# Kernel tuning notes

Hardware: AMD Instinct MI355X
Metric: run time of the kernel (lower is better)

The kernel has to match this reference:

```python
import jax, jax.numpy as jnp
import numpy as np

N_THRESHOLDS = 10


def setup_inputs() -> dict:
    key = jax.random.key(0)
    k1, k2, k3 = jax.random.split(key, 3)
    shape = (32, 1024, 1024)
    prediction = jax.random.normal(k1, shape, dtype=jnp.float32)
    mask = jax.random.randint(k2, shape, 0, 2, dtype=jnp.int32)
    target = jax.random.randint(k3, shape, 0, 2, dtype=jnp.int32)
    return {"prediction": prediction, "mask": mask, "target": target}


def reference(prediction, mask, target):
    # thresholds = linspace(0,1,n+2)[1:-1], same as the torch module
    thresholds = jnp.linspace(0.0, 1.0, N_THRESHOLDS + 2, dtype=jnp.float32)[1:-1]

    s = jax.nn.sigmoid(prediction).ravel()            # [N]
    m = mask.ravel().astype(bool)                     # [N] valid mask
    t = target.ravel().astype(bool)                   # [N]
    mt = m & t                                        # masked positives

    # Broadcast compare against all thresholds at once (single fused pass,
    # no per-threshold host sync like the original loop).
    pos = s[None, :] > thresholds[:, None]            # [T, N] bool

    tp = jnp.sum(pos & mt[None, :], axis=1)           # [T] int32
    p = jnp.sum(pos & m[None, :], axis=1)             # predicted-positive count

    total_m = jnp.sum(m)                              # total valid elements
    total_t = jnp.sum(mt)                             # total true positives in mask

    fp = p - tp
    fn = total_t - tp
    tn = total_m - p - fn

    # classes layout matches torch module: rows = [tp, fp, tn, fn]
    return jnp.stack([tp, fp, tn, fn], axis=0).astype(jnp.float32)
```

## Files before the change

kernel.cpp:

```cpp
#include <hip/hip_runtime.h>


#define NTHR 10
#define NBKT 11
#define NCNT 22
#define WS_STRIDE 16

typedef unsigned long long u64;
typedef unsigned u32;

typedef __attribute__((address_space(3))) void* lds_vp;
typedef const __attribute__((address_space(1))) void* gbl_vp;

__device__ __forceinline__ void ld_lds16(const void* g, void* l) {
    __builtin_amdgcn_global_load_lds((gbl_vp)g, (lds_vp)l, 16, 0, 0);
}

__device__ __forceinline__ unsigned wave_reduce_add(unsigned v) {
#pragma unroll
    for (int off = 32; off > 0; off >>= 1)
        v += __shfl_down(v, off, 64);
    return v;
}

__global__ __launch_bounds__(64) void zero_ws_kernel(u32* __restrict__ ws) {
    int i = threadIdx.x;
    if (i < NCNT) ws[i * WS_STRIDE] = 0u;
}

__device__ __forceinline__ void acc_elem(float x, u32 mm, u32 tt, u64& hP, u64& hT) {
    u32 mt = mm & tt;
    float e = __expf(-x);
    float s = __builtin_amdgcn_rcpf(1.0f + e);
    int bi = (int)(s * 11.0f);
    u32 b = (u32)(bi > 10 ? 10 : bi);
    u32 sh = b * 5u;
    hP += (u64)mm << sh;
    hT += (u64)mt << sh;
}

__device__ __forceinline__ void acc_vec(const float4& p, const int4& m, const int4& t,
                                        u64& hP, u64& hT) {
    acc_elem(p.x, (u32)m.x, (u32)t.x, hP, hT);
    acc_elem(p.y, (u32)m.y, (u32)t.y, hP, hT);
    acc_elem(p.z, (u32)m.z, (u32)t.z, hP, hT);
    acc_elem(p.w, (u32)m.w, (u32)t.w, hP, hT);
}

__device__ __forceinline__ void flush_hist(u64& hP, u64& hT,
                                           u64& Plo, u64& Phi, u64& Tlo, u64& Thi) {
#pragma unroll
    for (int b = 0; b < 6; ++b) {
        Plo += (u64)((u32)(hP >> (5 * b)) & 31u) << (10 * b);
        Tlo += (u64)((u32)(hT >> (5 * b)) & 31u) << (10 * b);
    }
#pragma unroll
    for (int b = 6; b < NBKT; ++b) {
        Phi += (u64)((u32)(hP >> (5 * b)) & 31u) << (10 * (b - 6));
        Thi += (u64)((u32)(hT >> (5 * b)) & 31u) << (10 * (b - 6));
    }
    hP = 0ull; hT = 0ull;
}

__global__ __launch_bounds__(256) void count_kernel(
        const float4* __restrict__ pred4,
        const int4*  __restrict__ mask4,
        const int4*  __restrict__ targ4,
        const float* __restrict__ pred,
        const int*   __restrict__ mask,
        const int*   __restrict__ targ,
        u32* __restrict__ ws, int nvec, int n) {
    __shared__ __align__(16) unsigned char stage[4][2][3][1024];
    __shared__ u32 partial[4][NCNT];

    u64 Plo = 0ull, Phi = 0ull, Tlo = 0ull, Thi = 0ull;

    const int tid        = blockIdx.x * blockDim.x + threadIdx.x;
    const int lane       = threadIdx.x & 63;
    const int wv         = threadIdx.x >> 6;
    const int waveG      = tid >> 6;
    const int totalWaves = (gridDim.x * blockDim.x) >> 6;
    const int nchunks    = nvec >> 6;


    int c   = waveG;
    int buf = 0;
    if (c < nchunks) {
        int gb = c << 6;
        ld_lds16(pred4 + gb + lane, stage[wv][0][0]);
        ld_lds16(mask4 + gb + lane, stage[wv][0][1]);
        ld_lds16(targ4 + gb + lane, stage[wv][0][2]);
    }
    while (c < nchunks) {
        int cn = c + totalWaves;
        if (cn < nchunks) {
            int gb = cn << 6;
            ld_lds16(pred4 + gb + lane, stage[wv][buf ^ 1][0]);
            ld_lds16(mask4 + gb + lane, stage[wv][buf ^ 1][1]);
            ld_lds16(targ4 + gb + lane, stage[wv][buf ^ 1][2]);
        }
        const float4* lp = (const float4*)stage[wv][buf][0];
        const int4*   lm = (const int4*)  stage[wv][buf][1];
        const int4*   lt = (const int4*)  stage[wv][buf][2];
        float4 p = lp[lane];
        int4   m = lm[lane];
        int4   t = lt[lane];

        u64 hP = 0ull, hT = 0ull;
        acc_vec(p, m, t, hP, hT);
        flush_hist(hP, hT, Plo, Phi, Tlo, Thi);

        c = cn;
        buf ^= 1;
    }

    for (int g = (nchunks << 6) + tid; g < nvec; g += gridDim.x * blockDim.x) {
        u64 hP = 0ull, hT = 0ull;
        acc_vec(pred4[g], mask4[g], targ4[g], hP, hT);
        flush_hist(hP, hT, Plo, Phi, Tlo, Thi);
    }
    {
        int i = nvec * 4 + tid;
        if (i < n) {
            u64 hP = 0ull, hT = 0ull;
            acc_elem(pred[i], (u32)mask[i], (u32)targ[i], hP, hT);
            flush_hist(hP, hT, Plo, Phi, Tlo, Thi);
        }
    }

    u32 vals[NCNT];
#pragma unroll
    for (int b = 0; b < 6; ++b) {
        vals[b]        = (u32)(Plo >> (10 * b)) & 1023u;
        vals[NBKT + b] = (u32)(Tlo >> (10 * b)) & 1023u;
    }
#pragma unroll
    for (int b = 6; b < NBKT; ++b) {
        vals[b]        = (u32)(Phi >> (10 * (b - 6))) & 1023u;
        vals[NBKT + b] = (u32)(Thi >> (10 * (b - 6))) & 1023u;
    }
#pragma unroll
    for (int cc = 0; cc < NCNT; ++cc) vals[cc] = wave_reduce_add(vals[cc]);

    if (lane == 0) {
#pragma unroll
        for (int cc = 0; cc < NCNT; ++cc) partial[wv][cc] = vals[cc];
    }
    __syncthreads();
    if (threadIdx.x < NCNT) {
        u32 s = partial[0][threadIdx.x] + partial[1][threadIdx.x] +
                partial[2][threadIdx.x] + partial[3][threadIdx.x];
        atomicAdd(&ws[threadIdx.x * WS_STRIDE], s);
    }
}

__global__ __launch_bounds__(64) void finalize_kernel(const u32* __restrict__ ws,
                                                      float* __restrict__ out) {
    int j = threadIdx.x;
    if (j < NTHR) {
        u32 totM = 0u, totT = 0u, p = 0u, tp = 0u;
#pragma unroll
        for (int b = 0; b < NBKT; ++b) {
            u32 vP = ws[b * WS_STRIDE];
            u32 vT = ws[(NBKT + b) * WS_STRIDE];
            totM += vP; totT += vT;
            if (b > j) { p += vP; tp += vT; }
        }
        u32 fp = p - tp;
        u32 fn = totT - tp;
        u32 tn = totM - p - fn;
        out[j]            = (float)tp;
        out[NTHR + j]     = (float)fp;
        out[2 * NTHR + j] = (float)tn;
        out[3 * NTHR + j] = (float)fn;
    }
}

extern "C" void kernel_launch(void* const* d_in, const int* in_sizes, int n_in,
                              void* d_out, int out_size, void* d_ws, size_t ws_size,
                              hipStream_t stream) {
    const float* pred = (const float*)d_in[0];
    const int*   mask = (const int*)d_in[1];
    const int*   targ = (const int*)d_in[2];
    u32*         ws   = (u32*)d_ws;
    float*       out  = (float*)d_out;

    const int n    = in_sizes[0];
    const int nvec = n / 4;

    zero_ws_kernel<<<1, 64, 0, stream>>>(ws);

    const int blocks = 2048;
    count_kernel<<<blocks, 256, 0, stream>>>(
        (const float4*)pred, (const int4*)mask, (const int4*)targ,
        pred, mask, targ, ws, nvec, n);

    finalize_kernel<<<1, 64, 0, stream>>>(ws, out);
}
```

Measured before the change: 359.8 us.

## Replace LDS async staging with direct unrolled global vector loads

Drops the double-buffered global_load_lds staging through shared memory. Each wave now issues twelve 16-byte global loads per iteration straight into registers, covering four 64-lane chunks. This keeps more memory requests in flight and removes the LDS round trip. It also packs 16 elements into each 5-bit-field histogram before flushing, which costs more live registers and makes loop-trip counts depend on grid size.

```diff
diff --git a/kernel.cpp b/kernel.cpp
--- a/kernel.cpp
+++ b/kernel.cpp
@@ -8,13 +8,6 @@
 
 typedef unsigned long long u64;
 typedef unsigned u32;
-
-typedef __attribute__((address_space(3))) void* lds_vp;
-typedef const __attribute__((address_space(1))) void* gbl_vp;
-
-__device__ __forceinline__ void ld_lds16(const void* g, void* l) {
-    __builtin_amdgcn_global_load_lds((gbl_vp)g, (lds_vp)l, 16, 0, 0);
-}
 
 __device__ __forceinline__ unsigned wave_reduce_add(unsigned v) {
 #pragma unroll
@@ -70,55 +63,44 @@
         const int*   __restrict__ mask,
         const int*   __restrict__ targ,
         u32* __restrict__ ws, int nvec, int n) {
-    __shared__ __align__(16) unsigned char stage[4][2][3][1024];
-    __shared__ u32 partial[4][NCNT];
-
     u64 Plo = 0ull, Phi = 0ull, Tlo = 0ull, Thi = 0ull;
 
-    const int tid        = blockIdx.x * blockDim.x + threadIdx.x;
-    const int lane       = threadIdx.x & 63;
-    const int wv         = threadIdx.x >> 6;
-    const int waveG      = tid >> 6;
+    const int tid    = blockIdx.x * blockDim.x + threadIdx.x;
+    const int lane   = tid & 63;
+    const int waveId = tid >> 6;
     const int totalWaves = (gridDim.x * blockDim.x) >> 6;
-    const int nchunks    = nvec >> 6;
+    const int strideG    = totalWaves << 8;
 
-
-    int c   = waveG;
-    int buf = 0;
-    if (c < nchunks) {
-        int gb = c << 6;
-        ld_lds16(pred4 + gb + lane, stage[wv][0][0]);
-        ld_lds16(mask4 + gb + lane, stage[wv][0][1]);
-        ld_lds16(targ4 + gb + lane, stage[wv][0][2]);
-    }
-    while (c < nchunks) {
-        int cn = c + totalWaves;
-        if (cn < nchunks) {
-            int gb = cn << 6;
-            ld_lds16(pred4 + gb + lane, stage[wv][buf ^ 1][0]);
-            ld_lds16(mask4 + gb + lane, stage[wv][buf ^ 1][1]);
-            ld_lds16(targ4 + gb + lane, stage[wv][buf ^ 1][2]);
+    for (int base = waveId << 8; base < nvec; base += strideG) {
+        u64 hP = 0ull, hT = 0ull;
+        if (base + 256 <= nvec) {
+            float4 p0 = pred4[base +        lane];
+            float4 p1 = pred4[base +  64  + lane];
+            float4 p2 = pred4[base + 128  + lane];
+            float4 p3 = pred4[base + 192  + lane];
+            int4   m0 = mask4[base +        lane];
+            int4   m1 = mask4[base +  64  + lane];
+            int4   m2 = mask4[base + 128  + lane];
+            int4   m3 = mask4[base + 192  + lane];
+            int4   t0 = targ4[base +        lane];
+            int4   t1 = targ4[base +  64  + lane];
+            int4   t2 = targ4[base + 128  + lane];
+            int4   t3 = targ4[base + 192  + lane];
+            acc_vec(p0, m0, t0, hP, hT);
+            acc_vec(p1, m1, t1, hP, hT);
+            acc_vec(p2, m2, t2, hP, hT);
+            acc_vec(p3, m3, t3, hP, hT);
+        } else {
+#pragma unroll
+            for (int c = 0; c < 4; ++c) {
+                int g = base + (c << 6) + lane;
+                if (g < nvec)
+                    acc_vec(pred4[g], mask4[g], targ4[g], hP, hT);
+            }
         }
-        const float4* lp = (const float4*)stage[wv][buf][0];
-        const int4*   lm = (const int4*)  stage[wv][buf][1];
-        const int4*   lt = (const int4*)  stage[wv][buf][2];
-        float4 p = lp[lane];
-        int4   m = lm[lane];
-        int4   t = lt[lane];
-
-        u64 hP = 0ull, hT = 0ull;
-        acc_vec(p, m, t, hP, hT);
         flush_hist(hP, hT, Plo, Phi, Tlo, Thi);
-
-        c = cn;
-        buf ^= 1;
     }
 
-    for (int g = (nchunks << 6) + tid; g < nvec; g += gridDim.x * blockDim.x) {
-        u64 hP = 0ull, hT = 0ull;
-        acc_vec(pred4[g], mask4[g], targ4[g], hP, hT);
-        flush_hist(hP, hT, Plo, Phi, Tlo, Thi);
-    }
     {
         int i = nvec * 4 + tid;
         if (i < n) {
@@ -140,11 +122,13 @@
         vals[NBKT + b] = (u32)(Thi >> (10 * (b - 6))) & 1023u;
     }
 #pragma unroll
-    for (int cc = 0; cc < NCNT; ++cc) vals[cc] = wave_reduce_add(vals[cc]);
+    for (int c = 0; c < NCNT; ++c) vals[c] = wave_reduce_add(vals[c]);
 
-    if (lane == 0) {
+    __shared__ u32 partial[4][NCNT];
+    const int wave = threadIdx.x >> 6;
+    if ((threadIdx.x & 63) == 0) {
 #pragma unroll
-        for (int cc = 0; cc < NCNT; ++cc) partial[wv][cc] = vals[cc];
+        for (int c = 0; c < NCNT; ++c) partial[wave][c] = vals[c];
     }
     __syncthreads();
     if (threadIdx.x < NCNT) {
```

After: 353.1 us. No clear change (-1.9%).
